# Optimization experiments

Hardware: AMD Instinct MI355X
Metric: run time of the kernel (lower is better)

The kernel has to match this reference:

```python
import jax, jax.numpy as jnp
import numpy as np

NUM_QUBITS = 13
NUM_LAYERS = 2


def setup_inputs() -> dict:
    key = jax.random.key(0)
    k1, k2 = jax.random.split(key)
    x = jax.random.normal(k1, (512, 2 ** NUM_QUBITS), dtype=jnp.float32)
    weights = jax.random.normal(k2, (NUM_LAYERS, NUM_QUBITS, 3), dtype=jnp.float32)
    return {"x": x, "weights": weights}


def _rot_matrix(phi, theta, omega):
    # qml.Rot(phi, theta, omega) = RZ(omega) @ RY(theta) @ RZ(phi)
    c = jnp.cos(theta * 0.5).astype(jnp.complex64)
    s = jnp.sin(theta * 0.5).astype(jnp.complex64)
    e_m = jnp.exp((-0.5j) * (phi + omega).astype(jnp.complex64))
    e_p = jnp.exp((0.5j) * (phi + omega).astype(jnp.complex64))
    e_d = jnp.exp((0.5j) * (phi - omega).astype(jnp.complex64))
    e_dc = jnp.exp((-0.5j) * (phi - omega).astype(jnp.complex64))
    row0 = jnp.stack([e_m * c, -e_d * s])
    row1 = jnp.stack([e_dc * s, e_p * c])
    return jnp.stack([row0, row1])  # (2, 2) complex64


def _apply_1q(psi, U, q):
    # psi: (B, 2, 2, ..., 2); contract qubit axis q with 2x2 gate U
    ax = 1 + q
    psi = jnp.moveaxis(psi, ax, -1)
    psi = psi @ U.T
    return jnp.moveaxis(psi, -1, ax)


def _apply_cnot(psi, c, t):
    # X on target where control bit == 1
    s0 = jax.lax.index_in_dim(psi, 0, axis=1 + c, keepdims=True)
    s1 = jax.lax.index_in_dim(psi, 1, axis=1 + c, keepdims=True)
    s1 = jnp.flip(s1, axis=1 + t)
    return jnp.concatenate([s0, s1], axis=1 + c)


def reference(x, weights):
    n = NUM_QUBITS
    B = x.shape[0]
    # AmplitudeEmbedding with normalize=True
    norm = jnp.sqrt(jnp.sum(x * x, axis=1, keepdims=True))
    psi = (x / norm).astype(jnp.complex64).reshape((B,) + (2,) * n)
    # StronglyEntanglingLayers (default ranges r_l = (l % (n-1)) + 1, CNOT imprimitive)
    for l in range(NUM_LAYERS):
        r = (l % (n - 1)) + 1
        for q in range(n):
            U = _rot_matrix(weights[l, q, 0], weights[l, q, 1], weights[l, q, 2])
            psi = _apply_1q(psi, U, q)
        for q in range(n):
            psi = _apply_cnot(psi, q, (q + r) % n)
    # expval(PauliZ(n // 2)) = p(bit=0) - p(bit=1)
    m = n // 2
    probs = jnp.real(psi) ** 2 + jnp.imag(psi) ** 2
    axes = tuple(i for i in range(1, n + 1) if i != 1 + m)
    p = probs.sum(axis=axes)  # (B, 2)
    return p[:, 0] - p[:, 1]
```

## Files before the change

kernel.cpp:

```cpp
#include <hip/hip_runtime.h>
#include <math.h>

#define NQ    13
#define DIM   8192
#define BLOCK 512
#define NGATE 26

__device__ __forceinline__ int SWZ(int i) {
    return i ^ (((((i >> 4) ^ (i >> 6)) & 3)) << 2)
             ^ ((((i >> 10) ^ (i >> 11)) & 1) << 4);
}

struct PCols { int c[NQ]; };
constexpr PCols make_cols(int r) {
    PCols P{};
    for (int b = 0; b < NQ; ++b) {
        int cc = 1 << b;
        for (int cq = 0; cq < NQ; ++cq) {
            const int cb = 12 - cq;
            const int tb = 12 - ((cq + r) % NQ);
            cc ^= ((cc >> cb) & 1) << tb;
        }
        P.c[b] = cc;
    }
    return P;
}
constexpr PCols C1 = make_cols(1);
constexpr int make_rm6() {
    int m = 0;
    for (int b = 0; b < NQ; ++b) m |= ((make_cols(2).c[b] >> 6) & 1) << b;
    return m;
}
constexpr int RM6 = make_rm6();

struct Combos { int k[16]; };
constexpr Combos make_combos() {
    Combos K{};
    for (int j = 0; j < 16; ++j)
        K.k[j] = ((j & 1) ? C1.c[0] : 0) ^ ((j & 2) ? C1.c[1] : 0)
               ^ ((j & 4) ? C1.c[2] : 0) ^ ((j & 8) ? C1.c[12] : 0);
    return K;
}
constexpr Combos KC = make_combos();

struct G8 { float4 a, b; };

template<int P>
__device__ __forceinline__ void rot16(float* vr, float* vi, const G8 g) {
    #pragma unroll
    for (int m = 0; m < 8; ++m) {
        const int j0 = ((m >> P) << (P + 1)) | (m & ((1 << P) - 1));
        const int j1 = j0 | (1 << P);
        const float a0r = vr[j0], a0i = vi[j0];
        const float a1r = vr[j1], a1i = vi[j1];
        vr[j0] = g.a.x * a0r - g.a.y * a0i + g.a.z * a1r - g.a.w * a1i;
        vi[j0] = g.a.x * a0i + g.a.y * a0r + g.a.z * a1i + g.a.w * a1r;
        vr[j1] = g.b.x * a0r - g.b.y * a0i + g.b.z * a1r - g.b.w * a1i;
        vi[j1] = g.b.x * a0i + g.b.y * a0r + g.b.z * a1i + g.b.w * a1r;
    }
}

template<int CTRL>
__device__ __forceinline__ float dppx(float v) {
    return __int_as_float(
        __builtin_amdgcn_update_dpp(0, __float_as_int(v), CTRL, 0xf, 0xf, true));
}

template<int CTRL>
__device__ __forceinline__ void rotlane16(float* vr, float* vi, const G8 g, const bool hi) {
    const float Ar = hi ? g.b.z : g.a.x;
    const float Ai = hi ? g.b.w : g.a.y;
    const float Br = hi ? g.b.x : g.a.z;
    const float Bi = hi ? g.b.y : g.a.w;
    #pragma unroll
    for (int j = 0; j < 16; ++j) {
        const float pr = dppx<CTRL>(vr[j]);
        const float pi = dppx<CTRL>(vi[j]);
        const float orr = vr[j], oii = vi[j];
        vr[j] = Ar * orr - Ai * oii + Br * pr - Bi * pi;
        vi[j] = Ar * oii + Ai * orr + Br * pi + Bi * pr;
    }
}

__device__ __forceinline__ void passA(float* re, float* im, const G8* __restrict__ gw,
                                      const int l, const int t) {
    float vr[16], vi[16];
    const int base = t << 4;
    #pragma unroll
    for (int g = 0; g < 4; ++g) {
        const int a = SWZ(base + 4 * g);
        *(float4*)&vr[4 * g] = *(const float4*)&re[a];
        *(float4*)&vi[4 * g] = *(const float4*)&im[a];
    }
    rot16<0>(vr, vi, gw[l * 13 + 12]);
    rot16<1>(vr, vi, gw[l * 13 + 11]);
    rot16<2>(vr, vi, gw[l * 13 + 10]);
    rot16<3>(vr, vi, gw[l * 13 +  9]);
    rotlane16<0xB1>(vr, vi, gw[l * 13 + 8], (t & 1) != 0);
    rotlane16<0x4E>(vr, vi, gw[l * 13 + 7], (t & 2) != 0);
    #pragma unroll
    for (int g = 0; g < 4; ++g) {
        const int a = SWZ(base + 4 * g);
        *(float4*)&re[a] = *(const float4*)&vr[4 * g];
        *(float4*)&im[a] = *(const float4*)&vi[4 * g];
    }
}

__device__ __forceinline__ void passB(float* re, float* im, const G8* __restrict__ gw,
                                      const int l, const int t) {
    float vr[16], vi[16];
    const int base = ((t >> 8) << 12) | ((t & 3) << 10) | ((t >> 2) & 63);
    const int sb = SWZ(base);
    #pragma unroll
    for (int j = 0; j < 16; ++j) {
        const int a = sb ^ (j << 6) ^ ((j & 3) << 2);
        vr[j] = re[a]; vi[j] = im[a];
    }
    rot16<0>(vr, vi, gw[l * 13 + 6]);
    rot16<1>(vr, vi, gw[l * 13 + 5]);
    rot16<2>(vr, vi, gw[l * 13 + 4]);
    rot16<3>(vr, vi, gw[l * 13 + 3]);
    rotlane16<0xB1>(vr, vi, gw[l * 13 + 2], (t & 1) != 0);
    rotlane16<0x4E>(vr, vi, gw[l * 13 + 1], (t & 2) != 0);
    #pragma unroll
    for (int j = 0; j < 16; ++j) {
        const int a = sb ^ (j << 6) ^ ((j & 3) << 2);
        re[a] = vr[j]; im[a] = vi[j];
    }
}

__device__ __forceinline__ void passC_load(const float* re, const float* im,
                                           float* vr, float* vi, const int t) {
    #pragma unroll
    for (int h = 0; h < 2; ++h)
        #pragma unroll
        for (int k = 0; k < 2; ++k) {
            const int a = SWZ((h << 12) | (t << 3) | (k << 2));
            *(float4*)&vr[h * 8 + 4 * k] = *(const float4*)&re[a];
            *(float4*)&vi[h * 8 + 4 * k] = *(const float4*)&im[a];
        }
}

__global__ void prep_gates(const float* __restrict__ w, G8* __restrict__ gw) {
    const int t = threadIdx.x;
    if (t < NGATE) {
        const float phi = w[t * 3 + 0], theta = w[t * 3 + 1], omega = w[t * 3 + 2];
        float c, s;  sincosf(0.5f * theta, &s, &c);
        float sps, cps, sds, cds;
        sincosf(0.5f * (phi + omega), &sps, &cps);
        sincosf(0.5f * (phi - omega), &sds, &cds);
        G8 g;
        g.a = make_float4(cps * c, -sps * c, -cds * s, -sds * s);
        g.b = make_float4(cds * s, -sds * s,  cps * c,  sps * c);
        gw[t] = g;
    }
}

__global__ __launch_bounds__(BLOCK, 4) void qsim_kernel(
    const float* __restrict__ x,
    const G8* __restrict__ gw,
    float* __restrict__ out)
{
    __shared__ float re[DIM];
    __shared__ float im[DIM];
    __shared__ float red[BLOCK / 64];

    const int b = blockIdx.x;
    const int t = threadIdx.x;

    const float4* x4 = (const float4*)(x + (size_t)b * DIM);
    float ss = 0.f;
    #pragma unroll
    for (int k = 0; k < 4; ++k) {
        const int m = t + BLOCK * k;
        const int a = SWZ(4 * m);
        const float4 v = x4[m];
        *(float4*)&re[a] = v;
        *(float4*)&im[a] = make_float4(0.f, 0.f, 0.f, 0.f);
        ss += v.x * v.x + v.y * v.y + v.z * v.z + v.w * v.w;
    }
    #pragma unroll
    for (int off = 32; off > 0; off >>= 1) ss += __shfl_down(ss, off, 64);
    if ((t & 63) == 0) red[t >> 6] = ss;
    __syncthreads();
    float total = 0.f;
    #pragma unroll
    for (int i = 0; i < BLOCK / 64; ++i) total += red[i];

    float vr[16], vi[16];

    passA(re, im, gw, 0, t);
    __syncthreads();
    passB(re, im, gw, 0, t);
    __syncthreads();
    passC_load(re, im, vr, vi, t);
    rot16<3>(vr, vi, gw[0 * 13 + 0]);
    __syncthreads();
    {
        int tpart = 0;
        #pragma unroll
        for (int bb = 0; bb < 9; ++bb)
            if ((t >> bb) & 1) tpart ^= C1.c[3 + bb];
        #pragma unroll
        for (int j = 0; j < 16; ++j) {
            const int a = SWZ(tpart ^ KC.k[j]);
            re[a] = vr[j]; im[a] = vi[j];
        }
    }
    __syncthreads();

    passA(re, im, gw, 1, t);
    __syncthreads();
    passB(re, im, gw, 1, t);
    __syncthreads();
    passC_load(re, im, vr, vi, t);
    rot16<3>(vr, vi, gw[1 * 13 + 0]);

    float acc = 0.f;
    #pragma unroll
    for (int j = 0; j < 16; ++j) {
        const int i = ((j >> 3) << 12) | (t << 3) | (j & 7);
        const float p = vr[j] * vr[j] + vi[j] * vi[j];
        acc += (__popc(i & RM6) & 1) ? -p : p;
    }
    #pragma unroll
    for (int off = 32; off > 0; off >>= 1) acc += __shfl_down(acc, off, 64);
    __syncthreads();
    if ((t & 63) == 0) red[t >> 6] = acc;
    __syncthreads();
    if (t == 0) {
        float tot = 0.f;
        #pragma unroll
        for (int i = 0; i < BLOCK / 64; ++i) tot += red[i];
        out[b] = tot / total;
    }
}

extern "C" void kernel_launch(void* const* d_in, const int* in_sizes, int n_in,
                              void* d_out, int out_size, void* d_ws, size_t ws_size,
                              hipStream_t stream) {
    const float* x = (const float*)d_in[0];
    const float* w = (const float*)d_in[1];
    float* out = (float*)d_out;
    G8* gw = (G8*)d_ws;
    const int B = in_sizes[0] / DIM;
    prep_gates<<<1, 64, 0, stream>>>(w, gw);
    qsim_kernel<<<B, BLOCK, 0, stream>>>(x, (const G8*)gw, out);
}
```

Before: 90.96 us.

## Fuse gate prep into kernel, re-partition passes, switch to packed float2 math

Each block now computes the gate matrices itself into shared memory, which removes the separate prep_gates launch. The three-pass gate schedule is re-partitioned with new thread-to-index mappings and a simpler XOR swizzle. Amplitudes are held as interleaved complex float2 values with fma chains, likely aiming for packed FP32 math. The final parity sign is precomputed as a bitmask. This trades a second launch for redundant per-block trig work and a riskier new indexing scheme.

After: 85.40 us. -6.1%, faster.

```diff
diff --git a/kernel.cpp b/kernel.cpp
--- a/kernel.cpp
+++ b/kernel.cpp
@@ -6,10 +6,7 @@
 #define BLOCK 512
 #define NGATE 26
 
-__device__ __forceinline__ int SWZ(int i) {
-    return i ^ (((((i >> 4) ^ (i >> 6)) & 3)) << 2)
-             ^ ((((i >> 10) ^ (i >> 11)) & 1) << 4);
-}
+__device__ __forceinline__ int SW(int a) { return a ^ (((a >> 7) & 7) << 2); }
 
 struct PCols { int c[NQ]; };
 constexpr PCols make_cols(int r) {
@@ -38,25 +35,41 @@
     Combos K{};
     for (int j = 0; j < 16; ++j)
         K.k[j] = ((j & 1) ? C1.c[0] : 0) ^ ((j & 2) ? C1.c[1] : 0)
-               ^ ((j & 4) ? C1.c[2] : 0) ^ ((j & 8) ? C1.c[12] : 0);
+               ^ ((j & 4) ? C1.c[10] : 0) ^ ((j & 8) ? C1.c[11] : 0);
     return K;
 }
 constexpr Combos KC = make_combos();
 
-struct G8 { float4 a, b; };
+constexpr int make_sjw() {
+    int wv = 0;
+    for (int j = 0; j < 16; ++j) {
+        const int jm = (j & 3) | (((j >> 2) & 3) << 10);
+        wv |= (__builtin_popcount(jm & RM6) & 1) << j;
+    }
+    return wv;
+}
+constexpr int SJW = make_sjw();
+
+__device__ __forceinline__ float2 f2mul(float s, float2 a) {
+    return make_float2(s * a.x, s * a.y);
+}
+__device__ __forceinline__ float2 f2fma(float s, float2 a, float2 b) {
+    return make_float2(fmaf(s, a.x, b.x), fmaf(s, a.y, b.y));
+}
+__device__ __forceinline__ float2 fswap(float2 a) { return make_float2(-a.y, a.x); }
 
 template<int P>
-__device__ __forceinline__ void rot16(float* vr, float* vi, const G8 g) {
+__device__ __forceinline__ void rotp(float2* c, const float* __restrict__ g) {
+    const float ur00 = g[0], ui00 = g[1], ur01 = g[2], ui01 = g[3];
+    const float ur10 = g[4], ui10 = g[5], ur11 = g[6], ui11 = g[7];
     #pragma unroll
     for (int m = 0; m < 8; ++m) {
         const int j0 = ((m >> P) << (P + 1)) | (m & ((1 << P) - 1));
         const int j1 = j0 | (1 << P);
-        const float a0r = vr[j0], a0i = vi[j0];
-        const float a1r = vr[j1], a1i = vi[j1];
-        vr[j0] = g.a.x * a0r - g.a.y * a0i + g.a.z * a1r - g.a.w * a1i;
-        vi[j0] = g.a.x * a0i + g.a.y * a0r + g.a.z * a1i + g.a.w * a1r;
-        vr[j1] = g.b.x * a0r - g.b.y * a0i + g.b.z * a1r - g.b.w * a1i;
-        vi[j1] = g.b.x * a0i + g.b.y * a0r + g.b.z * a1i + g.b.w * a1r;
+        const float2 a0 = c[j0], a1 = c[j1];
+        const float2 s0 = fswap(a0), s1 = fswap(a1);
+        c[j0] = f2fma(ui01, s1, f2fma(ur01, a1, f2fma(ui00, s0, f2mul(ur00, a0))));
+        c[j1] = f2fma(ui11, s1, f2fma(ur11, a1, f2fma(ui10, s0, f2mul(ur10, a0))));
     }
 }
 
@@ -65,115 +78,63 @@
     return __int_as_float(
         __builtin_amdgcn_update_dpp(0, __float_as_int(v), CTRL, 0xf, 0xf, true));
 }
-
 template<int CTRL>
-__device__ __forceinline__ void rotlane16(float* vr, float* vi, const G8 g, const bool hi) {
-    const float Ar = hi ? g.b.z : g.a.x;
-    const float Ai = hi ? g.b.w : g.a.y;
-    const float Br = hi ? g.b.x : g.a.z;
-    const float Bi = hi ? g.b.y : g.a.w;
+__device__ __forceinline__ void rotlane(float2* c, const float* __restrict__ g, const bool hi) {
+    const float Ar = hi ? g[6] : g[0];
+    const float Ai = hi ? g[7] : g[1];
+    const float Br = hi ? g[4] : g[2];
+    const float Bi = hi ? g[5] : g[3];
     #pragma unroll
     for (int j = 0; j < 16; ++j) {
-        const float pr = dppx<CTRL>(vr[j]);
-        const float pi = dppx<CTRL>(vi[j]);
-        const float orr = vr[j], oii = vi[j];
-        vr[j] = Ar * orr - Ai * oii + Br * pr - Bi * pi;
-        vi[j] = Ar * oii + Ai * orr + Br * pi + Bi * pr;
-    }
-}
-
-__device__ __forceinline__ void passA(float* re, float* im, const G8* __restrict__ gw,
-                                      const int l, const int t) {
-    float vr[16], vi[16];
-    const int base = t << 4;
-    #pragma unroll
-    for (int g = 0; g < 4; ++g) {
-        const int a = SWZ(base + 4 * g);
-        *(float4*)&vr[4 * g] = *(const float4*)&re[a];
-        *(float4*)&vi[4 * g] = *(const float4*)&im[a];
-    }
-    rot16<0>(vr, vi, gw[l * 13 + 12]);
-    rot16<1>(vr, vi, gw[l * 13 + 11]);
-    rot16<2>(vr, vi, gw[l * 13 + 10]);
-    rot16<3>(vr, vi, gw[l * 13 +  9]);
-    rotlane16<0xB1>(vr, vi, gw[l * 13 + 8], (t & 1) != 0);
-    rotlane16<0x4E>(vr, vi, gw[l * 13 + 7], (t & 2) != 0);
-    #pragma unroll
-    for (int g = 0; g < 4; ++g) {
-        const int a = SWZ(base + 4 * g);
-        *(float4*)&re[a] = *(const float4*)&vr[4 * g];
-        *(float4*)&im[a] = *(const float4*)&vi[4 * g];
-    }
-}
-
-__device__ __forceinline__ void passB(float* re, float* im, const G8* __restrict__ gw,
-                                      const int l, const int t) {
-    float vr[16], vi[16];
-    const int base = ((t >> 8) << 12) | ((t & 3) << 10) | ((t >> 2) & 63);
-    const int sb = SWZ(base);
-    #pragma unroll
-    for (int j = 0; j < 16; ++j) {
-        const int a = sb ^ (j << 6) ^ ((j & 3) << 2);
-        vr[j] = re[a]; vi[j] = im[a];
-    }
-    rot16<0>(vr, vi, gw[l * 13 + 6]);
-    rot16<1>(vr, vi, gw[l * 13 + 5]);
-    rot16<2>(vr, vi, gw[l * 13 + 4]);
-    rot16<3>(vr, vi, gw[l * 13 + 3]);
-    rotlane16<0xB1>(vr, vi, gw[l * 13 + 2], (t & 1) != 0);
-    rotlane16<0x4E>(vr, vi, gw[l * 13 + 1], (t & 2) != 0);
-    #pragma unroll
-    for (int j = 0; j < 16; ++j) {
-        const int a = sb ^ (j << 6) ^ ((j & 3) << 2);
-        re[a] = vr[j]; im[a] = vi[j];
-    }
-}
-
-__device__ __forceinline__ void passC_load(const float* re, const float* im,
-                                           float* vr, float* vi, const int t) {
-    #pragma unroll
-    for (int h = 0; h < 2; ++h)
-        #pragma unroll
-        for (int k = 0; k < 2; ++k) {
-            const int a = SWZ((h << 12) | (t << 3) | (k << 2));
-            *(float4*)&vr[h * 8 + 4 * k] = *(const float4*)&re[a];
-            *(float4*)&vi[h * 8 + 4 * k] = *(const float4*)&im[a];
-        }
-}
-
-__global__ void prep_gates(const float* __restrict__ w, G8* __restrict__ gw) {
+        const float2 p  = make_float2(dppx<CTRL>(c[j].x), dppx<CTRL>(c[j].y));
+        const float2 so = fswap(c[j]), sp = fswap(p);
+        c[j] = f2fma(Bi, sp, f2fma(Br, p, f2fma(Ai, so, f2mul(Ar, c[j]))));
+    }
+}
+
+__device__ __forceinline__ void loadgrp(const float* re, const float* im, int a, float2* c) {
+    const float4 r = *(const float4*)&re[a];
+    const float4 i = *(const float4*)&im[a];
+    c[0] = make_float2(r.x, i.x); c[1] = make_float2(r.y, i.y);
+    c[2] = make_float2(r.z, i.z); c[3] = make_float2(r.w, i.w);
+}
+__device__ __forceinline__ void storegrp(float* re, float* im, int a, const float2* c) {
+    *(float4*)&re[a] = make_float4(c[0].x, c[1].x, c[2].x, c[3].x);
+    *(float4*)&im[a] = make_float4(c[0].y, c[1].y, c[2].y, c[3].y);
+}
+
+__global__ __launch_bounds__(BLOCK, 4) void qsim_kernel(
+    const float* __restrict__ x,
+    const float* __restrict__ w,
+    float* __restrict__ out)
+{
+    __shared__ __align__(16) float re[DIM];
+    __shared__ __align__(16) float im[DIM];
+    __shared__ float gm[NGATE * 8];
+    __shared__ float red[BLOCK / 64];
+
+    const int b = blockIdx.x;
     const int t = threadIdx.x;
+
     if (t < NGATE) {
         const float phi = w[t * 3 + 0], theta = w[t * 3 + 1], omega = w[t * 3 + 2];
-        float c, s;  sincosf(0.5f * theta, &s, &c);
+        float co, si;  sincosf(0.5f * theta, &si, &co);
         float sps, cps, sds, cds;
         sincosf(0.5f * (phi + omega), &sps, &cps);
         sincosf(0.5f * (phi - omega), &sds, &cds);
-        G8 g;
-        g.a = make_float4(cps * c, -sps * c, -cds * s, -sds * s);
-        g.b = make_float4(cds * s, -sds * s,  cps * c,  sps * c);
-        gw[t] = g;
-    }
-}
-
-__global__ __launch_bounds__(BLOCK, 4) void qsim_kernel(
-    const float* __restrict__ x,
-    const G8* __restrict__ gw,
-    float* __restrict__ out)
-{
-    __shared__ float re[DIM];
-    __shared__ float im[DIM];
-    __shared__ float red[BLOCK / 64];
-
-    const int b = blockIdx.x;
-    const int t = threadIdx.x;
+        float* g = &gm[t * 8];
+        g[0] =  cps * co;  g[1] = -sps * co;
+        g[2] = -cds * si;  g[3] = -sds * si;
+        g[4] =  cds * si;  g[5] = -sds * si;
+        g[6] =  cps * co;  g[7] =  sps * co;
+    }
 
     const float4* x4 = (const float4*)(x + (size_t)b * DIM);
     float ss = 0.f;
     #pragma unroll
     for (int k = 0; k < 4; ++k) {
         const int m = t + BLOCK * k;
-        const int a = SWZ(4 * m);
+        const int a = SW(4 * m);
         const float4 v = x4[m];
         *(float4*)&re[a] = v;
         *(float4*)&im[a] = make_float4(0.f, 0.f, 0.f, 0.f);
@@ -187,45 +148,68 @@
     #pragma unroll
     for (int i = 0; i < BLOCK / 64; ++i) total += red[i];
 
-    float vr[16], vi[16];
-
-    passA(re, im, gw, 0, t);
-    __syncthreads();
-    passB(re, im, gw, 0, t);
-    __syncthreads();
-    passC_load(re, im, vr, vi, t);
-    rot16<3>(vr, vi, gw[0 * 13 + 0]);
-    __syncthreads();
-    {
-        int tpart = 0;
-        #pragma unroll
-        for (int bb = 0; bb < 9; ++bb)
-            if ((t >> bb) & 1) tpart ^= C1.c[3 + bb];
-        #pragma unroll
-        for (int j = 0; j < 16; ++j) {
-            const int a = SWZ(tpart ^ KC.k[j]);
-            re[a] = vr[j]; im[a] = vi[j];
+    float2 c[16];
+
+    const int base2 = (((t >> 2) & 15) << 2) | ((t & 3) << 8) | (((t >> 6) & 7) << 10);
+    const int base3 = (((t >> 1) & 255) << 2) | ((t & 1) << 12);
+
+    #pragma unroll
+    for (int l = 0; l < 2; ++l) {
+        const float* G = gm + l * 13 * 8;
+
+        #pragma unroll
+        for (int g = 0; g < 4; ++g) loadgrp(re, im, SW((t << 4) | (g << 2)), &c[4 * g]);
+        rotp<0>(c, G + 12 * 8);
+        rotp<1>(c, G + 11 * 8);
+        rotp<2>(c, G + 10 * 8);
+        rotp<3>(c, G +  9 * 8);
+        rotlane<0xB1>(c, G + 8 * 8, (t & 1) != 0);
+        rotlane<0x4E>(c, G + 7 * 8, (t & 2) != 0);
+        #pragma unroll
+        for (int g = 0; g < 4; ++g) storegrp(re, im, SW((t << 4) | (g << 2)), &c[4 * g]);
+        __syncthreads();
+
+        #pragma unroll
+        for (int h = 0; h < 4; ++h) loadgrp(re, im, SW(base2 | (h << 6)), &c[4 * h]);
+        rotp<2>(c, G + 6 * 8);
+        rotp<3>(c, G + 5 * 8);
+        rotlane<0xB1>(c, G + 4 * 8, (t & 1) != 0);
+        rotlane<0x4E>(c, G + 3 * 8, (t & 2) != 0);
+        #pragma unroll
+        for (int h = 0; h < 4; ++h) storegrp(re, im, SW(base2 | (h << 6)), &c[4 * h]);
+        __syncthreads();
+
+        #pragma unroll
+        for (int h = 0; h < 4; ++h) loadgrp(re, im, SW(base3 | (h << 10)), &c[4 * h]);
+        __syncthreads();
+        rotp<2>(c, G + 2 * 8);
+        rotp<3>(c, G + 1 * 8);
+        rotlane<0xB1>(c, G + 0 * 8, (t & 1) != 0);
+
+        if (l == 0) {
+            int mb = 0;
+            if (t & 1) mb ^= C1.c[12];
+            #pragma unroll
+            for (int bb = 0; bb < 8; ++bb)
+                if ((t >> (bb + 1)) & 1) mb ^= C1.c[2 + bb];
+            #pragma unroll
+            for (int j = 0; j < 16; ++j) {
+                const int a = SW(mb ^ KC.k[j]);
+                re[a] = c[j].x; im[a] = c[j].y;
+            }
+            __syncthreads();
         }
     }
-    __syncthreads();
-
-    passA(re, im, gw, 1, t);
-    __syncthreads();
-    passB(re, im, gw, 1, t);
-    __syncthreads();
-    passC_load(re, im, vr, vi, t);
-    rot16<3>(vr, vi, gw[1 * 13 + 0]);
-
+
+    const int sbase = __popc(base3 & RM6) & 1;
     float acc = 0.f;
     #pragma unroll
     for (int j = 0; j < 16; ++j) {
-        const int i = ((j >> 3) << 12) | (t << 3) | (j & 7);
-        const float p = vr[j] * vr[j] + vi[j] * vi[j];
-        acc += (__popc(i & RM6) & 1) ? -p : p;
+        const float p = c[j].x * c[j].x + c[j].y * c[j].y;
+        acc += (sbase ^ ((SJW >> j) & 1)) ? -p : p;
     }
     #pragma unroll
     for (int off = 32; off > 0; off >>= 1) acc += __shfl_down(acc, off, 64);
-    __syncthreads();
     if ((t & 63) == 0) red[t >> 6] = acc;
     __syncthreads();
     if (t == 0) {
@@ -242,8 +226,6 @@
     const float* x = (const float*)d_in[0];
     const float* w = (const float*)d_in[1];
     float* out = (float*)d_out;
-    G8* gw = (G8*)d_ws;
     const int B = in_sizes[0] / DIM;
-    prep_gates<<<1, 64, 0, stream>>>(w, gw);
-    qsim_kernel<<<B, BLOCK, 0, stream>>>(x, (const G8*)gw, out);
-}
+    qsim_kernel<<<B, BLOCK, 0, stream>>>(x, w, out);
+}
```
